# Optimization experiments

Hardware: AMD Instinct MI355X
Metric: run time of the kernel (lower is better)

The kernel has to match this reference:

```python
import jax, jax.numpy as jnp
import numpy as np

B, D, C, S = 65536, 128, 10, 2
LAMBDA_E, LAMBDA_OD = 0.1, 0.036
GAMMA_E, GAMMA_OD = 2.0, 2.0
STEP_SIZE = 1000.0


def setup_inputs() -> dict:
    key = jax.random.key(0)
    ks = jax.random.split(key, 12)
    inp = {
        "mean_t": jax.random.normal(ks[0], (B, D), jnp.float32),
        "mean_s": jax.random.normal(ks[1], (B, D), jnp.float32),
        "log_std_t": jax.random.normal(ks[2], (B, D), jnp.float32),
        "log_std_s": jax.random.normal(ks[3], (B, D), jnp.float32),
        "y_zt": jax.random.normal(ks[4], (B, C), jnp.float32),
        "s_zt": jax.random.normal(ks[5], (B, S), jnp.float32),
        "eps_prior_t": jax.random.normal(ks[6], (B, D), jnp.float32),
        "eps_prior_s": jax.random.normal(ks[7], (B, D), jnp.float32),
        "eps_t": jax.random.normal(ks[8], (B, D), jnp.float32),
        "eps_s": jax.random.normal(ks[9], (B, D), jnp.float32),
        "target": jax.random.randint(ks[10], (B,), 0, C, jnp.int64),
        "current_step": 500,
    }
    return inp


def _kld_batchmean(log_p, t):
    # torch KLDivLoss(reduction='batchmean'): sum(t * (log t - log_p)) / batch
    return jnp.sum(t * (jnp.log(t) - log_p)) / t.shape[0]


def reference(mean_t, mean_s, log_std_t, log_std_s, y_zt, s_zt,
              eps_prior_t, eps_prior_s, eps_t, eps_s, target, current_step):
    # CIFAR10 branch: cross entropy on task logits
    logp_y = jax.nn.log_softmax(y_zt, axis=1)
    L_t = -jnp.mean(jnp.take_along_axis(logp_y, target[:, None], axis=1))

    # entropy loss on sensitive discriminator output
    sm = jax.nn.softmax(s_zt, axis=1)
    lsm = jax.nn.log_softmax(s_zt, axis=1)
    Loss_e = -jnp.sum(sm * lsm) / s_zt.shape[0]

    # prior samples: N(0, I) and N(1, I)  (mean_tensors(zeros, ones))
    prior_t = eps_prior_t            # mean 0
    prior_s = 1.0 + eps_prior_s      # mean 1

    # encoder samples: MVN(mean, diag(exp(log_std))) -> std = exp(0.5*log_std)
    # torch .sample() is non-differentiable -> stop_gradient
    enc_t = jax.lax.stop_gradient(mean_t + jnp.exp(0.5 * log_std_t) * eps_t)
    enc_s = jax.lax.stop_gradient(mean_s + jnp.exp(0.5 * log_std_s) * eps_s)

    L_zt = _kld_batchmean(jax.nn.log_softmax(prior_t, axis=1), jax.nn.softmax(enc_t, axis=1))
    L_zs = _kld_batchmean(jax.nn.log_softmax(prior_s, axis=1), jax.nn.softmax(enc_s, axis=1))

    frac = current_step / STEP_SIZE
    lam_e = LAMBDA_E * GAMMA_E ** frac
    lam_od = LAMBDA_OD * GAMMA_OD ** frac
    return L_t + lam_e * Loss_e + lam_od * (L_zt + L_zs)
```

## Files before the change

### kernel.cpp

```cpp
#include <hip/hip_runtime.h>
#include <hip/hip_bf16.h>
#include <math.h>

#define BATCH   65536
#define DIMD    128
#define NCLS    10
#define NSENS   2
#define NBLOCKS 2048

__device__ __forceinline__ float half32_max(float v) {
    #pragma unroll
    for (int m = 16; m >= 1; m >>= 1) v = fmaxf(v, __shfl_xor(v, m, 64));
    return v;
}

__device__ __forceinline__ float kl_row(float4 mu, float4 ls, float4 ep, float4 pr) {
    float e0 = mu.x + __expf(0.5f * ls.x) * ep.x;
    float e1 = mu.y + __expf(0.5f * ls.y) * ep.y;
    float e2 = mu.z + __expf(0.5f * ls.z) * ep.z;
    float e3 = mu.w + __expf(0.5f * ls.w) * ep.w;

    float me = fmaxf(fmaxf(e0, e1), fmaxf(e2, e3));
    float mp = fmaxf(fmaxf(pr.x, pr.y), fmaxf(pr.z, pr.w));
    #pragma unroll
    for (int m = 16; m >= 1; m >>= 1) {
        me = fmaxf(me, __shfl_xor(me, m, 64));
        mp = fmaxf(mp, __shfl_xor(mp, m, 64));
    }

    float xe0 = __expf(e0 - me), xe1 = __expf(e1 - me);
    float xe2 = __expf(e2 - me), xe3 = __expf(e3 - me);
    float xp0 = __expf(pr.x - mp), xp1 = __expf(pr.y - mp);
    float xp2 = __expf(pr.z - mp), xp3 = __expf(pr.w - mp);

    float Ze = xe0 + xe1 + xe2 + xe3;
    float Zp = xp0 + xp1 + xp2 + xp3;
    float S  = xe0 * (e0 - pr.x) + xe1 * (e1 - pr.y)
             + xe2 * (e2 - pr.z) + xe3 * (e3 - pr.w);
    #pragma unroll
    for (int m = 16; m >= 1; m >>= 1) {
        Ze += __shfl_xor(Ze, m, 64);
        Zp += __shfl_xor(Zp, m, 64);
        S  += __shfl_xor(S,  m, 64);
    }

    float lse_e = me + __logf(Ze);
    float lse_p = mp + __logf(Zp);
    return S / Ze - lse_e + lse_p;
}

__global__ __launch_bounds__(256) void crit_main(
    const float* __restrict__ mean_t,      const float* __restrict__ mean_s,
    const float* __restrict__ log_std_t,   const float* __restrict__ log_std_s,
    const float* __restrict__ y_zt,        const float* __restrict__ s_zt,
    const float* __restrict__ eps_prior_t, const float* __restrict__ eps_prior_s,
    const float* __restrict__ eps_t,       const float* __restrict__ eps_s,
    const int*   __restrict__ target,
    double*      __restrict__ ws_partial)
{
    const int tid  = threadIdx.x;
    const int lane = tid & 63;
    const int sub  = lane & 31;
    const int half = lane >> 5;
    const int gwave = blockIdx.x * 4 + (tid >> 6);
    const int totalWaves = gridDim.x * 4;
    const int nPairs = BATCH / 2;

    double acc_ce = 0.0, acc_H = 0.0, acc_kl = 0.0;

    for (int pair = gwave; pair < nPairs; pair += totalWaves) {
        const int fidx = pair * 64 + lane;

        float4 mu = ((const float4*)mean_t)[fidx];
        float4 ls = ((const float4*)log_std_t)[fidx];
        float4 ep = ((const float4*)eps_t)[fidx];
        float4 pr = ((const float4*)eps_prior_t)[fidx];
        float kl_t = kl_row(mu, ls, ep, pr);

        mu = ((const float4*)mean_s)[fidx];
        ls = ((const float4*)log_std_s)[fidx];
        ep = ((const float4*)eps_s)[fidx];
        pr = ((const float4*)eps_prior_s)[fidx];
        float kl_s = kl_row(mu, ls, ep, pr);

        if (sub == 0) {
            const int r = pair * 2 + half;

            const float* yr = y_zt + (size_t)r * NCLS;
            float2 y01 = *(const float2*)(yr + 0);
            float2 y23 = *(const float2*)(yr + 2);
            float2 y45 = *(const float2*)(yr + 4);
            float2 y67 = *(const float2*)(yr + 6);
            float2 y89 = *(const float2*)(yr + 8);
            float m = fmaxf(fmaxf(fmaxf(y01.x, y01.y), fmaxf(y23.x, y23.y)),
                            fmaxf(fmaxf(y45.x, y45.y),
                                  fmaxf(fmaxf(y67.x, y67.y), fmaxf(y89.x, y89.y))));
            float Z = __expf(y01.x - m) + __expf(y01.y - m)
                    + __expf(y23.x - m) + __expf(y23.y - m)
                    + __expf(y45.x - m) + __expf(y45.y - m)
                    + __expf(y67.x - m) + __expf(y67.y - m)
                    + __expf(y89.x - m) + __expf(y89.y - m);
            float lse = m + __logf(Z);
            int   t   = target[r];
            float yt  = yr[t];
            float ce  = lse - yt;

            float2 s2 = *(const float2*)(s_zt + (size_t)r * NSENS);
            float ms  = fmaxf(s2.x, s2.y);
            float za  = __expf(s2.x - ms), zb = __expf(s2.y - ms);
            float Zs  = za + zb;
            float lses = ms + __logf(Zs);
            float pa = za / Zs, pb = zb / Zs;
            float H  = -(pa * (s2.x - lses) + pb * (s2.y - lses));

            acc_ce += (double)ce;
            acc_H  += (double)H;
            acc_kl += (double)kl_t + (double)kl_s;
        }
    }

    __shared__ double sh[8][3];
    if (sub == 0) {
        const int slot = tid >> 5;
        sh[slot][0] = acc_ce;
        sh[slot][1] = acc_H;
        sh[slot][2] = acc_kl;
    }
    __syncthreads();
    if (tid == 0) {
        double c = 0.0, h = 0.0, k = 0.0;
        #pragma unroll
        for (int i = 0; i < 8; ++i) { c += sh[i][0]; h += sh[i][1]; k += sh[i][2]; }
        ws_partial[blockIdx.x * 3 + 0] = c;
        ws_partial[blockIdx.x * 3 + 1] = h;
        ws_partial[blockIdx.x * 3 + 2] = k;
    }
}

__global__ __launch_bounds__(256) void crit_reduce(
    const double* __restrict__ ws_partial,
    const int*    __restrict__ step_ptr,
    float*        __restrict__ out,
    int nblocks)
{
    const int tid = threadIdx.x;
    double c = 0.0, h = 0.0, k = 0.0;
    for (int i = tid; i < nblocks; i += 256) {
        c += ws_partial[3 * i + 0];
        h += ws_partial[3 * i + 1];
        k += ws_partial[3 * i + 2];
    }
    __shared__ double sc[256], sh_[256], sk[256];
    sc[tid] = c; sh_[tid] = h; sk[tid] = k;
    __syncthreads();
    for (int s = 128; s > 0; s >>= 1) {
        if (tid < s) { sc[tid] += sc[tid + s]; sh_[tid] += sh_[tid + s]; sk[tid] += sk[tid + s]; }
        __syncthreads();
    }
    if (tid == 0) {
        double frac  = (double)step_ptr[0] / 1000.0;
        double lam_e  = 0.1   * exp2(frac);
        double lam_od = 0.036 * exp2(frac);
        out[0] = (float)((sc[0] + lam_e * sh_[0] + lam_od * sk[0]) / (double)BATCH);
    }
}

extern "C" void kernel_launch(void* const* d_in, const int* in_sizes, int n_in,
                              void* d_out, int out_size, void* d_ws, size_t ws_size,
                              hipStream_t stream) {
    const float* mean_t      = (const float*)d_in[0];
    const float* mean_s      = (const float*)d_in[1];
    const float* log_std_t   = (const float*)d_in[2];
    const float* log_std_s   = (const float*)d_in[3];
    const float* y_zt        = (const float*)d_in[4];
    const float* s_zt        = (const float*)d_in[5];
    const float* eps_prior_t = (const float*)d_in[6];
    const float* eps_prior_s = (const float*)d_in[7];
    const float* eps_t       = (const float*)d_in[8];
    const float* eps_s       = (const float*)d_in[9];
    const int*   target      = (const int*)d_in[10];
    const int*   step_ptr    = (const int*)d_in[11];

    double* ws_partial = (double*)d_ws;
    float*  out        = (float*)d_out;

    crit_main<<<NBLOCKS, 256, 0, stream>>>(
        mean_t, mean_s, log_std_t, log_std_s, y_zt, s_zt,
        eps_prior_t, eps_prior_s, eps_t, eps_s, target, ws_partial);
    crit_reduce<<<1, 256, 0, stream>>>(ws_partial, step_ptr, out, NBLOCKS);
}
```

Baseline: 266.4 us.

## Prefetch next pair, drop max-subtraction in softmax, batch warp reductions

Each wave now handles a fixed block of four row pairs and prefetches the next pair's eight float4 inputs and target while computing the current one, which hides memory latency. The max-subtraction shuffles are removed, so exps are taken directly on the inputs, and six warp reductions are interleaved in a single shuffle loop. This cuts shuffle and ALU work but risks float overflow for large logits. It also assumes the grid exactly covers the batch (2048 blocks × 4 waves × 4 pairs).

After: 268.9 us. Within noise of the previous version (+0.9%).

```diff
diff --git a/kernel.cpp b/kernel.cpp
--- a/kernel.cpp
+++ b/kernel.cpp
@@ -3,51 +3,10 @@
 #include <math.h>
 
 #define BATCH   65536
-#define DIMD    128
 #define NCLS    10
-#define NSENS   2
 #define NBLOCKS 2048
-
-__device__ __forceinline__ float half32_max(float v) {
-    #pragma unroll
-    for (int m = 16; m >= 1; m >>= 1) v = fmaxf(v, __shfl_xor(v, m, 64));
-    return v;
-}
-
-__device__ __forceinline__ float kl_row(float4 mu, float4 ls, float4 ep, float4 pr) {
-    float e0 = mu.x + __expf(0.5f * ls.x) * ep.x;
-    float e1 = mu.y + __expf(0.5f * ls.y) * ep.y;
-    float e2 = mu.z + __expf(0.5f * ls.z) * ep.z;
-    float e3 = mu.w + __expf(0.5f * ls.w) * ep.w;
-
-    float me = fmaxf(fmaxf(e0, e1), fmaxf(e2, e3));
-    float mp = fmaxf(fmaxf(pr.x, pr.y), fmaxf(pr.z, pr.w));
-    #pragma unroll
-    for (int m = 16; m >= 1; m >>= 1) {
-        me = fmaxf(me, __shfl_xor(me, m, 64));
-        mp = fmaxf(mp, __shfl_xor(mp, m, 64));
-    }
-
-    float xe0 = __expf(e0 - me), xe1 = __expf(e1 - me);
-    float xe2 = __expf(e2 - me), xe3 = __expf(e3 - me);
-    float xp0 = __expf(pr.x - mp), xp1 = __expf(pr.y - mp);
-    float xp2 = __expf(pr.z - mp), xp3 = __expf(pr.w - mp);
-
-    float Ze = xe0 + xe1 + xe2 + xe3;
-    float Zp = xp0 + xp1 + xp2 + xp3;
-    float S  = xe0 * (e0 - pr.x) + xe1 * (e1 - pr.y)
-             + xe2 * (e2 - pr.z) + xe3 * (e3 - pr.w);
-    #pragma unroll
-    for (int m = 16; m >= 1; m >>= 1) {
-        Ze += __shfl_xor(Ze, m, 64);
-        Zp += __shfl_xor(Zp, m, 64);
-        S  += __shfl_xor(S,  m, 64);
-    }
-
-    float lse_e = me + __logf(Ze);
-    float lse_p = mp + __logf(Zp);
-    return S / Ze - lse_e + lse_p;
-}
+#define PAIRS_PER_WAVE 4
+
 
 __global__ __launch_bounds__(256) void crit_main(
     const float* __restrict__ mean_t,      const float* __restrict__ mean_s,
@@ -63,59 +22,111 @@
     const int sub  = lane & 31;
     const int half = lane >> 5;
     const int gwave = blockIdx.x * 4 + (tid >> 6);
-    const int totalWaves = gridDim.x * 4;
-    const int nPairs = BATCH / 2;
+    const int base  = gwave * PAIRS_PER_WAVE;
+
+    const float4* MT = (const float4*)mean_t;
+    const float4* LT = (const float4*)log_std_t;
+    const float4* ET = (const float4*)eps_t;
+    const float4* PT = (const float4*)eps_prior_t;
+    const float4* MS = (const float4*)mean_s;
+    const float4* LS = (const float4*)log_std_s;
+    const float4* ES = (const float4*)eps_s;
+    const float4* PS = (const float4*)eps_prior_s;
 
     double acc_ce = 0.0, acc_H = 0.0, acc_kl = 0.0;
 
-    for (int pair = gwave; pair < nPairs; pair += totalWaves) {
-        const int fidx = pair * 64 + lane;
-
-        float4 mu = ((const float4*)mean_t)[fidx];
-        float4 ls = ((const float4*)log_std_t)[fidx];
-        float4 ep = ((const float4*)eps_t)[fidx];
-        float4 pr = ((const float4*)eps_prior_t)[fidx];
-        float kl_t = kl_row(mu, ls, ep, pr);
-
-        mu = ((const float4*)mean_s)[fidx];
-        ls = ((const float4*)log_std_s)[fidx];
-        ep = ((const float4*)eps_s)[fidx];
-        pr = ((const float4*)eps_prior_s)[fidx];
-        float kl_s = kl_row(mu, ls, ep, pr);
-
+    float4 cur[8];
+    int tgt_cur = 0;
+    {
+        const int fidx = base * 64 + lane;
+        cur[0] = MT[fidx]; cur[1] = LT[fidx]; cur[2] = ET[fidx]; cur[3] = PT[fidx];
+        cur[4] = MS[fidx]; cur[5] = LS[fidx]; cur[6] = ES[fidx]; cur[7] = PS[fidx];
+        if (sub == 0) tgt_cur = target[base * 2 + half];
+    }
+
+    #pragma unroll
+    for (int i = 0; i < PAIRS_PER_WAVE; ++i) {
+        const int pair = base + i;
+
+        float4 nxt[8];
+        int tgt_nxt = 0;
+        if (i + 1 < PAIRS_PER_WAVE) {
+            const int fidx = (pair + 1) * 64 + lane;
+            nxt[0] = MT[fidx]; nxt[1] = LT[fidx]; nxt[2] = ET[fidx]; nxt[3] = PT[fidx];
+            nxt[4] = MS[fidx]; nxt[5] = LS[fidx]; nxt[6] = ES[fidx]; nxt[7] = PS[fidx];
+            if (sub == 0) tgt_nxt = target[(pair + 1) * 2 + half];
+        }
+
+        const int r = pair * 2 + half;
+        float2 y01, y23, y45, y67, y89, s2;
+        float  yt = 0.0f;
         if (sub == 0) {
-            const int r = pair * 2 + half;
-
             const float* yr = y_zt + (size_t)r * NCLS;
-            float2 y01 = *(const float2*)(yr + 0);
-            float2 y23 = *(const float2*)(yr + 2);
-            float2 y45 = *(const float2*)(yr + 4);
-            float2 y67 = *(const float2*)(yr + 6);
-            float2 y89 = *(const float2*)(yr + 8);
-            float m = fmaxf(fmaxf(fmaxf(y01.x, y01.y), fmaxf(y23.x, y23.y)),
-                            fmaxf(fmaxf(y45.x, y45.y),
-                                  fmaxf(fmaxf(y67.x, y67.y), fmaxf(y89.x, y89.y))));
-            float Z = __expf(y01.x - m) + __expf(y01.y - m)
-                    + __expf(y23.x - m) + __expf(y23.y - m)
-                    + __expf(y45.x - m) + __expf(y45.y - m)
-                    + __expf(y67.x - m) + __expf(y67.y - m)
-                    + __expf(y89.x - m) + __expf(y89.y - m);
-            float lse = m + __logf(Z);
-            int   t   = target[r];
-            float yt  = yr[t];
-            float ce  = lse - yt;
-
-            float2 s2 = *(const float2*)(s_zt + (size_t)r * NSENS);
-            float ms  = fmaxf(s2.x, s2.y);
-            float za  = __expf(s2.x - ms), zb = __expf(s2.y - ms);
-            float Zs  = za + zb;
-            float lses = ms + __logf(Zs);
-            float pa = za / Zs, pb = zb / Zs;
-            float H  = -(pa * (s2.x - lses) + pb * (s2.y - lses));
+            y01 = *(const float2*)(yr + 0);
+            y23 = *(const float2*)(yr + 2);
+            y45 = *(const float2*)(yr + 4);
+            y67 = *(const float2*)(yr + 6);
+            y89 = *(const float2*)(yr + 8);
+            s2  = *(const float2*)(s_zt + (size_t)r * 2);
+            yt  = yr[tgt_cur];
+        }
+
+        const float4 mu_t = cur[0], ls_t = cur[1], ep_t = cur[2], pr_t = cur[3];
+        const float4 mu_s = cur[4], ls_s = cur[5], ep_s = cur[6], pr_s = cur[7];
+
+        float et0 = fmaf(__expf(0.5f * ls_t.x), ep_t.x, mu_t.x);
+        float et1 = fmaf(__expf(0.5f * ls_t.y), ep_t.y, mu_t.y);
+        float et2 = fmaf(__expf(0.5f * ls_t.z), ep_t.z, mu_t.z);
+        float et3 = fmaf(__expf(0.5f * ls_t.w), ep_t.w, mu_t.w);
+        float es0 = fmaf(__expf(0.5f * ls_s.x), ep_s.x, mu_s.x);
+        float es1 = fmaf(__expf(0.5f * ls_s.y), ep_s.y, mu_s.y);
+        float es2 = fmaf(__expf(0.5f * ls_s.z), ep_s.z, mu_s.z);
+        float es3 = fmaf(__expf(0.5f * ls_s.w), ep_s.w, mu_s.w);
+
+        float xt0 = __expf(et0), xt1 = __expf(et1), xt2 = __expf(et2), xt3 = __expf(et3);
+        float xs0 = __expf(es0), xs1 = __expf(es1), xs2 = __expf(es2), xs3 = __expf(es3);
+
+        float red[6];
+        red[0] = (xt0 + xt1) + (xt2 + xt3);
+        red[1] = (__expf(pr_t.x) + __expf(pr_t.y)) + (__expf(pr_t.z) + __expf(pr_t.w));
+        red[2] = (xt0 * (et0 - pr_t.x) + xt1 * (et1 - pr_t.y))
+               + (xt2 * (et2 - pr_t.z) + xt3 * (et3 - pr_t.w));
+        red[3] = (xs0 + xs1) + (xs2 + xs3);
+        red[4] = (__expf(pr_s.x) + __expf(pr_s.y)) + (__expf(pr_s.z) + __expf(pr_s.w));
+        red[5] = (xs0 * (es0 - pr_s.x) + xs1 * (es1 - pr_s.y))
+               + (xs2 * (es2 - pr_s.z) + xs3 * (es3 - pr_s.w));
+
+        #pragma unroll
+        for (int m = 16; m >= 1; m >>= 1) {
+            #pragma unroll
+            for (int j = 0; j < 6; ++j) red[j] += __shfl_xor(red[j], m, 64);
+        }
+
+        const float rt = 1.0f / red[0];
+        const float rs = 1.0f / red[3];
+        const float kl = red[2] * rt + __logf(red[1] * rt)
+                       + red[5] * rs + __logf(red[4] * rs);
+
+        if (sub == 0) {
+            float Z = (__expf(y01.x) + __expf(y01.y)) + (__expf(y23.x) + __expf(y23.y))
+                    + (__expf(y45.x) + __expf(y45.y)) + (__expf(y67.x) + __expf(y67.y))
+                    + (__expf(y89.x) + __expf(y89.y));
+            float ce = __logf(Z) - yt;
+
+            float za = __expf(s2.x), zb = __expf(s2.y);
+            float Zs = za + zb;
+            float lses = __logf(Zs);
+            float H  = -((za / Zs) * (s2.x - lses) + (zb / Zs) * (s2.y - lses));
 
             acc_ce += (double)ce;
             acc_H  += (double)H;
-            acc_kl += (double)kl_t + (double)kl_s;
+            acc_kl += (double)kl;
+        }
+
+        if (i + 1 < PAIRS_PER_WAVE) {
+            #pragma unroll
+            for (int j = 0; j < 8; ++j) cur[j] = nxt[j];
+            tgt_cur = tgt_nxt;
         }
     }
 
```
